# Performance work log

Hardware: AMD Instinct MI355X
Metric: run time of the kernel (lower is better)

The kernel has to match this reference:

```python
import jax, jax.numpy as jnp
import numpy as np

SH, SW = 24, 24       # superpixel grid (num_spixels = 576)
R = 2                 # window_size=5 -> r=2
TEMP = 0.01
N_ITERS = 5
BIG = 1e16


def setup_inputs() -> dict:
    key = jax.random.key(0)
    pixel_features = jax.random.normal(key, (8, 96, 96, 384), dtype=jnp.float32)
    return {"pixel_features": pixel_features}


def _pairwise_dist(f1, f2):
    # f1: (B, C, N) pixels, f2: (B, C, M) superpixels -> (B, M, N)
    return (jnp.sum(f1 * f1, axis=1)[:, None, :]
            + jnp.sum(f2 * f2, axis=1)[:, :, None]
            - 2.0 * jnp.einsum('bcm,bcn->bmn', f2, f1))


def reference(pixel_features):
    B, H, W, C = pixel_features.shape
    M = SH * SW
    x = jnp.transpose(pixel_features, (0, 3, 1, 2))  # (B, C, H, W)

    # init centroids: adaptive_avg_pool2d with divisible dims == block mean
    cent = x.reshape(B, C, SH, H // SH, SW, W // SW).mean(axis=(3, 5)).reshape(B, C, M)

    # nearest-neighbor upsampled label map (same for all batches)
    row = (jnp.arange(H) * SH) // H  # floor(i*SH/H), matches torch 'nearest'
    col = (jnp.arange(W) * SW) // W
    label_map = (row[:, None] * SW + col[None, :]).reshape(-1)  # (N,)

    spix = jnp.arange(M)
    rel_w = label_map[None, :] % SW - spix[:, None] % SW        # (M, N)
    rel_h = label_map[None, :] // SW - spix[:, None] // SW
    mask = (jnp.abs(rel_w) <= R) & (jnp.abs(rel_h) <= R)
    mask_dist = jnp.where(mask, 0.0, BIG).astype(jnp.float32)   # (M, N)

    pix = x.reshape(B, C, H * W)                # (B, C, N)
    pixT = jnp.transpose(pix, (0, 2, 1))        # (B, N, C)

    sp = cent
    for _ in range(N_ITERS):
        d = _pairwise_dist(pix, sp) + mask_dist[None]          # (B, M, N)
        aff = jax.lax.stop_gradient(jax.nn.softmax(-d * TEMP, axis=1))
        sp_new = jnp.einsum('bmn,bnc->bmc', aff, pixT)          # (B, M, C)
        sp_new = sp_new / jnp.maximum(aff.sum(axis=2, keepdims=True), 1e-16)
        sp = jnp.transpose(sp_new, (0, 2, 1))                   # (B, C, M)

    d = _pairwise_dist(pix, sp)
    hard_labels = jnp.argmin(d, axis=1)                         # (B, N)
    spixel_features = jnp.transpose(sp, (0, 2, 1)).reshape(B, SH, SW, C)
    return spixel_features, hard_labels
```

## Files before the change

### kernel.cpp

```cpp
#include <hip/hip_runtime.h>

#define B_ 8
#define H_ 96
#define W_ 96
#define C_ 384
#define SH_ 24
#define SW_ 24
#define M_ 576
#define N_ 9216
#define TEMP_ 0.01f

__global__ __launch_bounds__(384) void k_init(const float* __restrict__ pix,
                                              float* __restrict__ sp,
                                              float* __restrict__ sq) {
  int bm = blockIdx.x;
  int b = bm / M_, m = bm % M_;
  int mh = m / SW_, mw = m % SW_;
  int c = threadIdx.x;
  const float* base = pix + (((size_t)(b * H_ + mh * 4)) * W_ + mw * 4) * C_ + c;
  float s = 0.f;
#pragma unroll
  for (int i = 0; i < 4; i++)
#pragma unroll
    for (int j = 0; j < 4; j++)
      s += base[(size_t)(i * W_ + j) * C_];
  s *= 0.0625f;
  sp[((size_t)(b * M_) + m) * C_ + c] = s;
  float q = s * s;
#pragma unroll
  for (int off = 32; off > 0; off >>= 1) q += __shfl_down(q, off);
  __shared__ float red[6];
  if ((c & 63) == 0) red[c >> 6] = q;
  __syncthreads();
  if (c == 0) sq[b * M_ + m] = red[0] + red[1] + red[2] + red[3] + red[4] + red[5];
}

__global__ __launch_bounds__(128) void k_aff(const float* __restrict__ pix,
                                             const float* __restrict__ sp,
                                             const float* __restrict__ sq,
                                             float* __restrict__ aff) {
  int wg = blockIdx.x;
  int b = wg / 72, r = wg % 72;
  int lh = r / 3, lw0 = (r % 3) * 8;
  __shared__ float sL[60 * 196];
  __shared__ float sqL[60];
  int t = threadIdx.x;
  for (int e = t; e < 60; e += 128) {
    int mh = lh - 2 + e / 12, mw = lw0 - 2 + e % 12;
    sqL[e] = (mh >= 0 && mh < SH_ && mw >= 0 && mw < SW_) ? sq[b * M_ + mh * SW_ + mw] : 0.f;
  }
  int i = t >> 4, j = t & 15;
  int lw = lw0 + i;
  int h = lh * 4 + (j >> 2), w = lw * 4 + (j & 3);
  const float* prow = pix + (((size_t)(b * H_ + h)) * W_ + w) * C_;
  float acc[25];
#pragma unroll
  for (int k = 0; k < 25; k++) acc[k] = 0.f;

  for (int half = 0; half < 2; half++) {
    __syncthreads();
    int cbase = half * 192;
    for (int e = t; e < 60 * 48; e += 128) {
      int u = e / 48, c4 = e % 48;
      int mh = lh - 2 + u / 12, mw = lw0 - 2 + u % 12;
      float4 v = make_float4(0.f, 0.f, 0.f, 0.f);
      if (mh >= 0 && mh < SH_ && mw >= 0 && mw < SW_)
        v = *(const float4*)(sp + ((size_t)(b * M_ + mh * SW_ + mw)) * C_ + cbase + c4 * 4);
      *(float4*)&sL[u * 196 + c4 * 4] = v;
    }
    __syncthreads();
    for (int c0 = 0; c0 < 192; c0 += 8) {
      float4 pa = *(const float4*)(prow + cbase + c0);
      float4 pb = *(const float4*)(prow + cbase + c0 + 4);
#pragma unroll
      for (int dh = 0; dh < 5; dh++) {
#pragma unroll
        for (int dw = 0; dw < 5; dw++) {
          const float* srow = &sL[(dh * 12 + i + dw) * 196 + c0];
          float4 sa = *(const float4*)srow;
          float4 sb = *(const float4*)(srow + 4);
          float tsum = fmaf(pa.x, sa.x, fmaf(pa.y, sa.y, fmaf(pa.z, sa.z, pa.w * sa.w)));
          tsum = fmaf(pb.x, sb.x, fmaf(pb.y, sb.y, fmaf(pb.z, sb.z, fmaf(pb.w, sb.w, tsum))));
          acc[dh * 5 + dw] += tsum;
        }
      }
    }
  }
  float lg[25];
  float mx = -3e38f;
#pragma unroll
  for (int dh = 0; dh < 5; dh++) {
#pragma unroll
    for (int dw = 0; dw < 5; dw++) {
      int k = dh * 5 + dw;
      int mh = lh - 2 + dh, mw = lw - 2 + dw;
      int u = dh * 12 + i + dw;
      bool valid = (mh >= 0) && (mh < SH_) && (mw >= 0) && (mw < SW_);
      float l = valid ? (TEMP_ * (2.f * acc[k] - sqL[u])) : -3e38f;
      lg[k] = l;
      mx = fmaxf(mx, l);
    }
  }
  float z = 0.f;
#pragma unroll
  for (int k = 0; k < 25; k++) {
    float e = __expf(lg[k] - mx);
    lg[k] = e;
    z += e;
  }
  float inv = 1.f / z;
  float* arow = aff + ((size_t)(b * N_) + h * W_ + w) * 25;
#pragma unroll
  for (int k = 0; k < 25; k++) arow[k] = lg[k] * inv;
}

__global__ __launch_bounds__(384) void k_scatter(const float* __restrict__ pix,
                                                 const float* __restrict__ aff,
                                                 float* __restrict__ accum) {
  int wg = blockIdx.x;
  int b = wg / 48, r = wg % 48;
  int lh = r / 2, lw0 = (r % 2) * 12;
  int c = threadIdx.x;
  float acc[5][16];
#pragma unroll
  for (int a = 0; a < 5; a++)
#pragma unroll
    for (int w2 = 0; w2 < 16; w2++) acc[a][w2] = 0.f;
#pragma unroll
  for (int lwl = 0; lwl < 12; lwl++) {
    int lw = lw0 + lwl;
#pragma unroll 4
    for (int jj = 0; jj < 16; jj++) {
      int h = lh * 4 + (jj >> 2);
      int w = lw * 4 + (jj & 3);
      const float* ar = aff + ((size_t)(b * N_) + h * W_ + w) * 25;
      float val = pix[(((size_t)(b * H_) + h) * W_ + w) * C_ + c];
#pragma unroll
      for (int dh = 0; dh < 5; dh++)
#pragma unroll
        for (int dw = 0; dw < 5; dw++)
          acc[dh][lwl + dw] = fmaf(ar[dh * 5 + dw], val, acc[dh][lwl + dw]);
    }
  }
#pragma unroll
  for (int dh = 0; dh < 5; dh++) {
    int mh = lh - 2 + dh;
    if (mh < 0 || mh >= SH_) continue;
#pragma unroll
    for (int wi = 0; wi < 16; wi++) {
      int mw = lw0 - 2 + wi;
      if (mw < 0 || mw >= SW_) continue;
      atomicAdd(&accum[((size_t)(b * M_) + mh * SW_ + mw) * C_ + c], acc[dh][wi]);
    }
  }
}

__global__ __launch_bounds__(384) void k_fin(const float* __restrict__ aff,
                                             const float* __restrict__ accum,
                                             float* __restrict__ sp,
                                             float* __restrict__ sq) {
  int bm = blockIdx.x;
  int b = bm / M_, m = bm % M_;
  int mh = m / SW_, mw = m % SW_;
  int t = threadIdx.x;
  int h0 = (mh - 2) * 4; if (h0 < 0) h0 = 0;
  int h1 = (mh + 3) * 4; if (h1 > H_) h1 = H_;
  int w0 = (mw - 2) * 4; if (w0 < 0) w0 = 0;
  int w1 = (mw + 3) * 4; if (w1 > W_) w1 = W_;
  int nw = w1 - w0;
  int np = (h1 - h0) * nw;
  float d = 0.f;
  for (int e = t; e < np; e += 384) {
    int hh = h0 + e / nw, ww = w0 + e % nw;
    int k = (mh - (hh >> 2) + 2) * 5 + (mw - (ww >> 2) + 2);
    d += aff[((size_t)(b * N_) + hh * W_ + ww) * 25 + k];
  }
  __shared__ float red[6];
#pragma unroll
  for (int off = 32; off > 0; off >>= 1) d += __shfl_down(d, off);
  if ((t & 63) == 0) red[t >> 6] = d;
  __syncthreads();
  float denom = fmaxf(red[0] + red[1] + red[2] + red[3] + red[4] + red[5], 1e-16f);
  size_t idx = ((size_t)(b * M_) + m) * C_ + t;
  float sv = accum[idx] / denom;
  sp[idx] = sv;
  float q = sv * sv;
#pragma unroll
  for (int off = 32; off > 0; off >>= 1) q += __shfl_down(q, off);
  __syncthreads();
  if ((t & 63) == 0) red[t >> 6] = q;
  __syncthreads();
  if (t == 0) sq[b * M_ + m] = red[0] + red[1] + red[2] + red[3] + red[4] + red[5];
}

__global__ __launch_bounds__(256) void k_argmin(const float* __restrict__ pix,
                                                const float* __restrict__ sp,
                                                const float* __restrict__ sq,
                                                float* __restrict__ lab) {
  int wg = blockIdx.x;
  int b = wg / 72;
  int px0 = (wg % 72) * 128;
  __shared__ float pT[128 * 36];
  __shared__ float sT[64 * 36];
  __shared__ float sqT[64];
  int t = threadIdx.x;
  int pxg = t >> 4, cg = t & 15;
  float best[8];
  int bidx[8];
#pragma unroll
  for (int x = 0; x < 8; x++) { best[x] = 3.4e38f; bidx[x] = 0; }

  for (int m0 = 0; m0 < M_; m0 += 64) {
    __syncthreads();
    if (t < 64) sqT[t] = sq[b * M_ + m0 + t];
    float acc[8][4];
#pragma unroll
    for (int x = 0; x < 8; x++)
#pragma unroll
      for (int y = 0; y < 4; y++) acc[x][y] = 0.f;

    for (int k0 = 0; k0 < C_; k0 += 32) {
      __syncthreads();
      {
        int row = t >> 1, o = (t & 1) * 16;
        const float* src = pix + ((size_t)(b * N_) + px0 + row) * C_ + k0 + o;
        int sw = (row >> 3) & 7;
#pragma unroll
        for (int jj = 0; jj < 4; jj++) {
          float4 v = *(const float4*)(src + jj * 4);
          int ob = (o >> 2) + jj;
          *(float4*)&pT[row * 36 + ((ob ^ sw) << 2)] = v;
        }
      }
      if (t < 128) {
        int row = t >> 1, o = (t & 1) * 16;
        const float* src = sp + ((size_t)(b * M_) + m0 + row) * C_ + k0 + o;
        int sw = (row >> 2) & 7;
#pragma unroll
        for (int jj = 0; jj < 4; jj++) {
          float4 v = *(const float4*)(src + jj * 4);
          int ob = (o >> 2) + jj;
          *(float4*)&sT[row * 36 + ((ob ^ sw) << 2)] = v;
        }
      }
      __syncthreads();
#pragma unroll
      for (int q = 0; q < 8; q++) {
        float4 bb[4];
#pragma unroll
        for (int y = 0; y < 4; y++) {
          int row = (cg << 2) + y;
          bb[y] = *(const float4*)&sT[row * 36 + ((q ^ (cg & 7)) << 2)];
        }
#pragma unroll
        for (int x = 0; x < 8; x++) {
          int row = (pxg << 3) + x;
          float4 av = *(const float4*)&pT[row * 36 + ((q ^ (pxg & 7)) << 2)];
#pragma unroll
          for (int y = 0; y < 4; y++) {
            acc[x][y] = fmaf(av.x, bb[y].x,
                        fmaf(av.y, bb[y].y,
                        fmaf(av.z, bb[y].z,
                        fmaf(av.w, bb[y].w, acc[x][y]))));
          }
        }
      }
    }
#pragma unroll
    for (int y = 0; y < 4; y++) {
      int mi = m0 + (cg << 2) + y;
      float dq = sqT[(cg << 2) + y];
#pragma unroll
      for (int x = 0; x < 8; x++) {
        float dist = dq - 2.f * acc[x][y];
        if (dist < best[x]) { best[x] = dist; bidx[x] = mi; }
      }
    }
  }
#pragma unroll
  for (int off = 1; off < 16; off <<= 1) {
#pragma unroll
    for (int x = 0; x < 8; x++) {
      float ov = __shfl_xor(best[x], off, 16);
      int oi = __shfl_xor(bidx[x], off, 16);
      if (ov < best[x] || (ov == best[x] && oi < bidx[x])) { best[x] = ov; bidx[x] = oi; }
    }
  }
  if (cg == 0) {
#pragma unroll
    for (int x = 0; x < 8; x++)
      lab[(size_t)(b * N_) + px0 + (pxg << 3) + x] = (float)bidx[x];
  }
}

__global__ __launch_bounds__(256) void k_copy(const float4* __restrict__ src,
                                              float4* __restrict__ dst) {
  int i = blockIdx.x * 256 + threadIdx.x;
  dst[i] = src[i];
}

extern "C" void kernel_launch(void* const* d_in, const int* in_sizes, int n_in,
                              void* d_out, int out_size, void* d_ws, size_t ws_size,
                              hipStream_t stream) {
  const float* pix = (const float*)d_in[0];
  float* out = (float*)d_out;
  char* ws = (char*)d_ws;
  float* sp    = (float*)(ws);
  float* accum = (float*)(ws + 7077888);
  float* aff   = (float*)(ws + 14155776);
  float* sq    = (float*)(ws + 21528576);

  k_init<<<B_ * M_, 384, 0, stream>>>(pix, sp, sq);
  for (int it = 0; it < 5; it++) {
    hipMemsetAsync(accum, 0, 7077888, stream);
    k_aff<<<576, 128, 0, stream>>>(pix, sp, sq, aff);
    k_scatter<<<384, 384, 0, stream>>>(pix, aff, accum);
    k_fin<<<B_ * M_, 384, 0, stream>>>(aff, accum, sp, sq);
  }
  k_argmin<<<576, 256, 0, stream>>>(pix, sp, sq, out + 1769472);
  k_copy<<<1728, 256, 0, stream>>>((const float4*)sp, (float4*)out);
}
```

Baseline: 1.742 ms.

## Split affinity and argmin kernels across channels and centroids with atomic reduction

The affinity kernel becomes k_dot, which splits the channel dimension into four quarters and processes two pixels per thread across a full superpixel row. Partial dot products are combined into a zeroed buffer with atomicAdd, and a separate k_soft kernel then applies the softmax. The final argmin is split over centroid tiles of 128, giving five times more blocks, and each block merges its result through a 64-bit atomicMin on a packed (distance, index) key held in the output buffer. A k_label pass then unpacks the indices. This raises parallelism for the two compute-heavy stages, at the cost of atomic traffic, an extra memset region and two extra launches.

After: 3.273 ms. 87.9% more time.

```diff
diff --git a/kernel.cpp b/kernel.cpp
--- a/kernel.cpp
+++ b/kernel.cpp
@@ -12,7 +12,10 @@
 
 __global__ __launch_bounds__(384) void k_init(const float* __restrict__ pix,
                                               float* __restrict__ sp,
-                                              float* __restrict__ sq) {
+                                              float* __restrict__ sq,
+                                              unsigned long long* __restrict__ lab64) {
+  int gid = blockIdx.x * 384 + threadIdx.x;
+  if (gid < N_ * B_) lab64[gid] = ~0ull;
   int bm = blockIdx.x;
   int b = bm / M_, m = bm % M_;
   int mh = m / SW_, mw = m % SW_;
@@ -35,68 +38,93 @@
   if (c == 0) sq[b * M_ + m] = red[0] + red[1] + red[2] + red[3] + red[4] + red[5];
 }
 
-__global__ __launch_bounds__(128) void k_aff(const float* __restrict__ pix,
+#define DOT8(ACC, A, BV, SA, SB)                                              \
+  ACC = fmaf((A).x, (SA).x, fmaf((A).y, (SA).y, fmaf((A).z, (SA).z,           \
+        fmaf((A).w, (SA).w, fmaf((BV).x, (SB).x, fmaf((BV).y, (SB).y,         \
+        fmaf((BV).z, (SB).z, fmaf((BV).w, (SB).w, ACC))))))))
+
+__global__ __launch_bounds__(192) void k_dot(const float* __restrict__ pix,
                                              const float* __restrict__ sp,
-                                             const float* __restrict__ sq,
-                                             float* __restrict__ aff) {
+                                             float* __restrict__ dotb) {
   int wg = blockIdx.x;
-  int b = wg / 72, r = wg % 72;
-  int lh = r / 3, lw0 = (r % 3) * 8;
-  __shared__ float sL[60 * 196];
-  __shared__ float sqL[60];
+  int b = wg / 96, r = wg % 96;
+  int lh = r >> 2, quarter = r & 3;
+  int qb = quarter * 96;
+  __shared__ float sL[120 * 52];
   int t = threadIdx.x;
-  for (int e = t; e < 60; e += 128) {
-    int mh = lh - 2 + e / 12, mw = lw0 - 2 + e % 12;
-    sqL[e] = (mh >= 0 && mh < SH_ && mw >= 0 && mw < SW_) ? sq[b * M_ + mh * SW_ + mw] : 0.f;
-  }
-  int i = t >> 4, j = t & 15;
-  int lw = lw0 + i;
-  int h = lh * 4 + (j >> 2), w = lw * 4 + (j & 3);
-  const float* prow = pix + (((size_t)(b * H_ + h)) * W_ + w) * C_;
-  float acc[25];
-#pragma unroll
-  for (int k = 0; k < 25; k++) acc[k] = 0.f;
-
-  for (int half = 0; half < 2; half++) {
+  int lw = t >> 3, pp = t & 7;
+  int h1 = lh * 4 + (pp >> 2), w1 = lw * 4 + (pp & 3);
+  int h2 = h1 + 2;
+  const float* p1 = pix + (((size_t)(b * H_ + h1)) * W_ + w1) * C_ + qb;
+  const float* p2 = pix + (((size_t)(b * H_ + h2)) * W_ + w1) * C_ + qb;
+  int mwc[5];
+#pragma unroll
+  for (int dw = 0; dw < 5; dw++) {
+    int v = lw - 2 + dw;
+    mwc[dw] = v < 0 ? 0 : (v > 23 ? 23 : v);
+  }
+  float acc0[25], acc1[25];
+#pragma unroll
+  for (int k = 0; k < 25; k++) { acc0[k] = 0.f; acc1[k] = 0.f; }
+
+  for (int stg = 0; stg < 2; stg++) {
     __syncthreads();
-    int cbase = half * 192;
-    for (int e = t; e < 60 * 48; e += 128) {
-      int u = e / 48, c4 = e % 48;
-      int mh = lh - 2 + u / 12, mw = lw0 - 2 + u % 12;
+    int cb = stg * 48;
+    for (int e = t; e < 120 * 12; e += 192) {
+      int u = e / 12, c4 = e % 12;
+      int mh = lh - 2 + u / 24, mw = u % 24;
       float4 v = make_float4(0.f, 0.f, 0.f, 0.f);
-      if (mh >= 0 && mh < SH_ && mw >= 0 && mw < SW_)
-        v = *(const float4*)(sp + ((size_t)(b * M_ + mh * SW_ + mw)) * C_ + cbase + c4 * 4);
-      *(float4*)&sL[u * 196 + c4 * 4] = v;
+      if (mh >= 0 && mh < SH_)
+        v = *(const float4*)(sp + ((size_t)(b * M_ + mh * SW_ + mw)) * C_ + qb + cb + c4 * 4);
+      *(float4*)&sL[u * 52 + c4 * 4] = v;
     }
     __syncthreads();
-    for (int c0 = 0; c0 < 192; c0 += 8) {
-      float4 pa = *(const float4*)(prow + cbase + c0);
-      float4 pb = *(const float4*)(prow + cbase + c0 + 4);
+    for (int c0 = 0; c0 < 48; c0 += 8) {
+      float4 a0 = *(const float4*)(p1 + cb + c0);
+      float4 b0 = *(const float4*)(p1 + cb + c0 + 4);
+      float4 a1 = *(const float4*)(p2 + cb + c0);
+      float4 b1 = *(const float4*)(p2 + cb + c0 + 4);
 #pragma unroll
       for (int dh = 0; dh < 5; dh++) {
 #pragma unroll
         for (int dw = 0; dw < 5; dw++) {
-          const float* srow = &sL[(dh * 12 + i + dw) * 196 + c0];
+          const float* srow = &sL[(dh * 24 + mwc[dw]) * 52 + c0];
           float4 sa = *(const float4*)srow;
           float4 sb = *(const float4*)(srow + 4);
-          float tsum = fmaf(pa.x, sa.x, fmaf(pa.y, sa.y, fmaf(pa.z, sa.z, pa.w * sa.w)));
-          tsum = fmaf(pb.x, sb.x, fmaf(pb.y, sb.y, fmaf(pb.z, sb.z, fmaf(pb.w, sb.w, tsum))));
-          acc[dh * 5 + dw] += tsum;
+          int k = dh * 5 + dw;
+          DOT8(acc0[k], a0, b0, sa, sb);
+          DOT8(acc1[k], a1, b1, sa, sb);
         }
       }
     }
   }
+  float* d1 = dotb + ((size_t)(b * N_) + h1 * W_ + w1) * 25;
+  float* d2 = dotb + ((size_t)(b * N_) + h2 * W_ + w1) * 25;
+#pragma unroll
+  for (int k = 0; k < 25; k++) {
+    atomicAdd(d1 + k, acc0[k]);
+    atomicAdd(d2 + k, acc1[k]);
+  }
+}
+
+__global__ __launch_bounds__(256) void k_soft(float* __restrict__ buf,
+                                              const float* __restrict__ sq) {
+  int gid = blockIdx.x * 256 + threadIdx.x;
+  int b = gid / N_, rem = gid % N_;
+  int h = rem / W_, w = rem % W_;
+  int lh = h >> 2, lw = w >> 2;
+  float* row = buf + (size_t)gid * 25;
   float lg[25];
-  float mx = -3e38f;
+  float mx = -3.0e38f;
 #pragma unroll
   for (int dh = 0; dh < 5; dh++) {
 #pragma unroll
     for (int dw = 0; dw < 5; dw++) {
       int k = dh * 5 + dw;
-      int mh = lh - 2 + dh, mw = lw - 2 + dw;
-      int u = dh * 12 + i + dw;
+      int mh = lh + dh - 2, mw = lw + dw - 2;
       bool valid = (mh >= 0) && (mh < SH_) && (mw >= 0) && (mw < SW_);
-      float l = valid ? (TEMP_ * (2.f * acc[k] - sqL[u])) : -3e38f;
+      float l = -3.0e38f;
+      if (valid) l = TEMP_ * (2.f * row[k] - sq[b * M_ + mh * SW_ + mw]);
       lg[k] = l;
       mx = fmaxf(mx, l);
     }
@@ -109,9 +137,8 @@
     z += e;
   }
   float inv = 1.f / z;
-  float* arow = aff + ((size_t)(b * N_) + h * W_ + w) * 25;
-#pragma unroll
-  for (int k = 0; k < 25; k++) arow[k] = lg[k] * inv;
+#pragma unroll
+  for (int k = 0; k < 25; k++) row[k] = lg[k] * inv;
 }
 
 __global__ __launch_bounds__(384) void k_scatter(const float* __restrict__ pix,
@@ -196,85 +223,74 @@
 __global__ __launch_bounds__(256) void k_argmin(const float* __restrict__ pix,
                                                 const float* __restrict__ sp,
                                                 const float* __restrict__ sq,
-                                                float* __restrict__ lab) {
+                                                unsigned long long* __restrict__ lab64) {
   int wg = blockIdx.x;
-  int b = wg / 72;
-  int px0 = (wg % 72) * 128;
+  int b = wg / 360;
+  int r = wg % 360;
+  int px0 = (r / 5) * 128;
+  int m0 = (r % 5) * 128;
   __shared__ float pT[128 * 36];
-  __shared__ float sT[64 * 36];
-  __shared__ float sqT[64];
+  __shared__ float sT[128 * 36];
+  __shared__ float sqT[128];
   int t = threadIdx.x;
   int pxg = t >> 4, cg = t & 15;
+  if (t < 128) {
+    int mm = m0 + t;
+    sqT[t] = (mm < M_) ? sq[b * M_ + mm] : 3.0e38f;
+  }
+  float acc[8][8];
+#pragma unroll
+  for (int x = 0; x < 8; x++)
+#pragma unroll
+    for (int y = 0; y < 8; y++) acc[x][y] = 0.f;
+
+  int srow_ = t >> 1, so_ = (t & 1) * 16;
+  int ssw_ = (srow_ >> 3) & 7;
+  int mrow_ = m0 + srow_; if (mrow_ > M_ - 1) mrow_ = M_ - 1;
+  const float* psrc0 = pix + ((size_t)(b * N_) + px0 + srow_) * C_ + so_;
+  const float* ssrc0 = sp + ((size_t)(b * M_) + mrow_) * C_ + so_;
+
+  for (int k0 = 0; k0 < C_; k0 += 32) {
+    __syncthreads();
+#pragma unroll
+    for (int jj = 0; jj < 4; jj++) {
+      float4 v = *(const float4*)(psrc0 + k0 + jj * 4);
+      float4 u = *(const float4*)(ssrc0 + k0 + jj * 4);
+      int ob = (so_ >> 2) + jj;
+      *(float4*)&pT[srow_ * 36 + (((ob ^ ssw_) & 7) << 2)] = v;
+      *(float4*)&sT[srow_ * 36 + (((ob ^ ssw_) & 7) << 2)] = u;
+    }
+    __syncthreads();
+#pragma unroll
+    for (int q = 0; q < 8; q++) {
+      float4 bb[8];
+      int sb = (q ^ (cg & 7)) << 2;
+#pragma unroll
+      for (int y = 0; y < 8; y++)
+        bb[y] = *(const float4*)&sT[(cg * 8 + y) * 36 + sb];
+      int pb = (q ^ (pxg & 7)) << 2;
+#pragma unroll
+      for (int x = 0; x < 8; x++) {
+        float4 av = *(const float4*)&pT[(pxg * 8 + x) * 36 + pb];
+#pragma unroll
+        for (int y = 0; y < 8; y++)
+          acc[x][y] = fmaf(av.x, bb[y].x, fmaf(av.y, bb[y].y,
+                      fmaf(av.z, bb[y].z, fmaf(av.w, bb[y].w, acc[x][y]))));
+      }
+    }
+  }
   float best[8];
   int bidx[8];
 #pragma unroll
   for (int x = 0; x < 8; x++) { best[x] = 3.4e38f; bidx[x] = 0; }
-
-  for (int m0 = 0; m0 < M_; m0 += 64) {
-    __syncthreads();
-    if (t < 64) sqT[t] = sq[b * M_ + m0 + t];
-    float acc[8][4];
-#pragma unroll
-    for (int x = 0; x < 8; x++)
-#pragma unroll
-      for (int y = 0; y < 4; y++) acc[x][y] = 0.f;
-
-    for (int k0 = 0; k0 < C_; k0 += 32) {
-      __syncthreads();
-      {
-        int row = t >> 1, o = (t & 1) * 16;
-        const float* src = pix + ((size_t)(b * N_) + px0 + row) * C_ + k0 + o;
-        int sw = (row >> 3) & 7;
-#pragma unroll
-        for (int jj = 0; jj < 4; jj++) {
-          float4 v = *(const float4*)(src + jj * 4);
-          int ob = (o >> 2) + jj;
-          *(float4*)&pT[row * 36 + ((ob ^ sw) << 2)] = v;
-        }
-      }
-      if (t < 128) {
-        int row = t >> 1, o = (t & 1) * 16;
-        const float* src = sp + ((size_t)(b * M_) + m0 + row) * C_ + k0 + o;
-        int sw = (row >> 2) & 7;
-#pragma unroll
-        for (int jj = 0; jj < 4; jj++) {
-          float4 v = *(const float4*)(src + jj * 4);
-          int ob = (o >> 2) + jj;
-          *(float4*)&sT[row * 36 + ((ob ^ sw) << 2)] = v;
-        }
-      }
-      __syncthreads();
-#pragma unroll
-      for (int q = 0; q < 8; q++) {
-        float4 bb[4];
-#pragma unroll
-        for (int y = 0; y < 4; y++) {
-          int row = (cg << 2) + y;
-          bb[y] = *(const float4*)&sT[row * 36 + ((q ^ (cg & 7)) << 2)];
-        }
-#pragma unroll
-        for (int x = 0; x < 8; x++) {
-          int row = (pxg << 3) + x;
-          float4 av = *(const float4*)&pT[row * 36 + ((q ^ (pxg & 7)) << 2)];
-#pragma unroll
-          for (int y = 0; y < 4; y++) {
-            acc[x][y] = fmaf(av.x, bb[y].x,
-                        fmaf(av.y, bb[y].y,
-                        fmaf(av.z, bb[y].z,
-                        fmaf(av.w, bb[y].w, acc[x][y]))));
-          }
-        }
-      }
-    }
-#pragma unroll
-    for (int y = 0; y < 4; y++) {
-      int mi = m0 + (cg << 2) + y;
-      float dq = sqT[(cg << 2) + y];
-#pragma unroll
-      for (int x = 0; x < 8; x++) {
-        float dist = dq - 2.f * acc[x][y];
-        if (dist < best[x]) { best[x] = dist; bidx[x] = mi; }
-      }
+#pragma unroll
+  for (int y = 0; y < 8; y++) {
+    int m = m0 + cg * 8 + y;
+    float dq = sqT[cg * 8 + y];
+#pragma unroll
+    for (int x = 0; x < 8; x++) {
+      float d = dq - 2.f * acc[x][y];
+      if (d < best[x]) { best[x] = d; bidx[x] = m; }
     }
   }
 #pragma unroll
@@ -288,9 +304,19 @@
   }
   if (cg == 0) {
 #pragma unroll
-    for (int x = 0; x < 8; x++)
-      lab[(size_t)(b * N_) + px0 + (pxg << 3) + x] = (float)bidx[x];
-  }
+    for (int x = 0; x < 8; x++) {
+      unsigned u = __float_as_uint(best[x]);
+      unsigned k32 = (u & 0x80000000u) ? ~u : (u | 0x80000000u);
+      unsigned long long key = ((unsigned long long)k32 << 32) | (unsigned)bidx[x];
+      atomicMin(lab64 + (size_t)b * N_ + px0 + pxg * 8 + x, key);
+    }
+  }
+}
+
+__global__ __launch_bounds__(256) void k_label(const unsigned long long* __restrict__ lab64,
+                                               float* __restrict__ lab) {
+  int i = blockIdx.x * 256 + threadIdx.x;
+  lab[i] = (float)(unsigned)(lab64[i] & 0xFFFFFFFFull);
 }
 
 __global__ __launch_bounds__(256) void k_copy(const float4* __restrict__ src,
@@ -307,16 +333,19 @@
   char* ws = (char*)d_ws;
   float* sp    = (float*)(ws);
   float* accum = (float*)(ws + 7077888);
-  float* aff   = (float*)(ws + 14155776);
+  float* buf   = (float*)(ws + 14155776);
   float* sq    = (float*)(ws + 21528576);
-
-  k_init<<<B_ * M_, 384, 0, stream>>>(pix, sp, sq);
+  unsigned long long* lab64 = (unsigned long long*)d_out;
+
+  k_init<<<B_ * M_, 384, 0, stream>>>(pix, sp, sq, lab64);
   for (int it = 0; it < 5; it++) {
-    hipMemsetAsync(accum, 0, 7077888, stream);
-    k_aff<<<576, 128, 0, stream>>>(pix, sp, sq, aff);
-    k_scatter<<<384, 384, 0, stream>>>(pix, aff, accum);
-    k_fin<<<B_ * M_, 384, 0, stream>>>(aff, accum, sp, sq);
-  }
-  k_argmin<<<576, 256, 0, stream>>>(pix, sp, sq, out + 1769472);
+    hipMemsetAsync(accum, 0, 7077888 + 7372800, stream);
+    k_dot<<<768, 192, 0, stream>>>(pix, sp, buf);
+    k_soft<<<288, 256, 0, stream>>>(buf, sq);
+    k_scatter<<<384, 384, 0, stream>>>(pix, buf, accum);
+    k_fin<<<B_ * M_, 384, 0, stream>>>(buf, accum, sp, sq);
+  }
+  k_argmin<<<2880, 256, 0, stream>>>(pix, sp, sq, lab64);
+  k_label<<<288, 256, 0, stream>>>(lab64, out + 1769472);
   k_copy<<<1728, 256, 0, stream>>>((const float4*)sp, (float4*)out);
 }
```

## Split argmin over superpixel tiles with 64-bit atomicMin and shrink k_aff LDS

Applied to the files above, without the earlier changes.

k_argmin now splits the superpixel dimension into 5 tiles of 128, so it launches 2880 workgroups instead of 576. It uses 8x8 register tiles per thread with register-prefetch double buffering, and merges partial argmins through a 64-bit atomicMin on packed (distance key, index) values. A new k_label kernel unpacks those keys into float labels, and k_init clears the 64-bit buffer, which lives temporarily in the output area. k_aff stages centroid data in 48-channel chunks instead of 192, cutting its shared memory to raise occupancy at the cost of more barriers. Risks: the atomic traffic, the extra pass, and the 64-bit buffer aliasing the output region that k_copy writes later.

Measured after the change: 1.744 ms. About the same (+0.1%).

```diff
diff --git a/kernel.cpp b/kernel.cpp
--- a/kernel.cpp
+++ b/kernel.cpp
@@ -12,7 +12,10 @@
 
 __global__ __launch_bounds__(384) void k_init(const float* __restrict__ pix,
                                               float* __restrict__ sp,
-                                              float* __restrict__ sq) {
+                                              float* __restrict__ sq,
+                                              unsigned long long* __restrict__ lab64) {
+  int gid = blockIdx.x * 384 + threadIdx.x;
+  if (gid < N_ * B_) lab64[gid] = ~0ull;
   int bm = blockIdx.x;
   int b = bm / M_, m = bm % M_;
   int mh = m / SW_, mw = m % SW_;
@@ -42,7 +45,7 @@
   int wg = blockIdx.x;
   int b = wg / 72, r = wg % 72;
   int lh = r / 3, lw0 = (r % 3) * 8;
-  __shared__ float sL[60 * 196];
+  __shared__ float sL[60 * 52];
   __shared__ float sqL[60];
   int t = threadIdx.x;
   for (int e = t; e < 60; e += 128) {
@@ -57,26 +60,27 @@
 #pragma unroll
   for (int k = 0; k < 25; k++) acc[k] = 0.f;
 
-  for (int half = 0; half < 2; half++) {
+  for (int chunk = 0; chunk < 8; chunk++) {
+    int cb = chunk * 48;
     __syncthreads();
-    int cbase = half * 192;
-    for (int e = t; e < 60 * 48; e += 128) {
-      int u = e / 48, c4 = e % 48;
+    for (int e = t; e < 60 * 12; e += 128) {
+      int u = e / 12, c4 = e % 12;
       int mh = lh - 2 + u / 12, mw = lw0 - 2 + u % 12;
       float4 v = make_float4(0.f, 0.f, 0.f, 0.f);
       if (mh >= 0 && mh < SH_ && mw >= 0 && mw < SW_)
-        v = *(const float4*)(sp + ((size_t)(b * M_ + mh * SW_ + mw)) * C_ + cbase + c4 * 4);
-      *(float4*)&sL[u * 196 + c4 * 4] = v;
+        v = *(const float4*)(sp + ((size_t)(b * M_ + mh * SW_ + mw)) * C_ + cb + c4 * 4);
+      *(float4*)&sL[u * 52 + c4 * 4] = v;
     }
     __syncthreads();
-    for (int c0 = 0; c0 < 192; c0 += 8) {
-      float4 pa = *(const float4*)(prow + cbase + c0);
-      float4 pb = *(const float4*)(prow + cbase + c0 + 4);
+#pragma unroll
+    for (int c0 = 0; c0 < 48; c0 += 8) {
+      float4 pa = *(const float4*)(prow + cb + c0);
+      float4 pb = *(const float4*)(prow + cb + c0 + 4);
 #pragma unroll
       for (int dh = 0; dh < 5; dh++) {
 #pragma unroll
         for (int dw = 0; dw < 5; dw++) {
-          const float* srow = &sL[(dh * 12 + i + dw) * 196 + c0];
+          const float* srow = &sL[(dh * 12 + i + dw) * 52 + c0];
           float4 sa = *(const float4*)srow;
           float4 sb = *(const float4*)(srow + 4);
           float tsum = fmaf(pa.x, sa.x, fmaf(pa.y, sa.y, fmaf(pa.z, sa.z, pa.w * sa.w)));
@@ -196,101 +200,118 @@
 __global__ __launch_bounds__(256) void k_argmin(const float* __restrict__ pix,
                                                 const float* __restrict__ sp,
                                                 const float* __restrict__ sq,
-                                                float* __restrict__ lab) {
+                                                unsigned long long* __restrict__ lab64) {
   int wg = blockIdx.x;
-  int b = wg / 72;
-  int px0 = (wg % 72) * 128;
+  int b = wg / 360;
+  int r = wg % 360;
+  int px0 = (r / 5) * 128;
+  int m0 = (r % 5) * 128;
   __shared__ float pT[128 * 36];
-  __shared__ float sT[64 * 36];
-  __shared__ float sqT[64];
+  __shared__ float sT[128 * 36];
+  __shared__ float sqT[128];
   int t = threadIdx.x;
-  int pxg = t >> 4, cg = t & 15;
+  int wave = t >> 6, lane = t & 63;
+  int wpx = wave >> 1, wc = wave & 1;
+  int pxg = lane >> 3, cg = lane & 7;
+  if (t < 128) {
+    int mm = m0 + t;
+    sqT[t] = (mm < M_) ? sq[b * M_ + mm] : 3.0e38f;
+  }
+  int srow = t >> 1;
+  int sslot0 = (t & 1) * 4;
+  int ssw = (srow >> 3) & 7;
+  int mrow = m0 + srow; if (mrow > M_ - 1) mrow = M_ - 1;
+  const float* psrc = pix + ((size_t)(b * N_) + px0 + srow) * C_ + sslot0 * 4;
+  const float* ssrc = sp + ((size_t)(b * M_) + mrow) * C_ + sslot0 * 4;
+  float* pdst = &pT[srow * 36];
+  float* sdst = &sT[srow * 36];
+
+  float acc[8][8];
+#pragma unroll
+  for (int x = 0; x < 8; x++)
+#pragma unroll
+    for (int y = 0; y < 8; y++) acc[x][y] = 0.f;
+
+  float4 pr[4], sr[4];
+#pragma unroll
+  for (int jj = 0; jj < 4; jj++) {
+    pr[jj] = *(const float4*)(psrc + jj * 4);
+    sr[jj] = *(const float4*)(ssrc + jj * 4);
+  }
+
+  for (int k0 = 0; k0 < C_; k0 += 32) {
+    __syncthreads();
+#pragma unroll
+    for (int jj = 0; jj < 4; jj++) {
+      int slot = (sslot0 + jj) ^ ssw;
+      *(float4*)&pdst[slot << 2] = pr[jj];
+      *(float4*)&sdst[slot << 2] = sr[jj];
+    }
+    __syncthreads();
+    if (k0 + 32 < C_) {
+#pragma unroll
+      for (int jj = 0; jj < 4; jj++) {
+        pr[jj] = *(const float4*)(psrc + k0 + 32 + jj * 4);
+        sr[jj] = *(const float4*)(ssrc + k0 + 32 + jj * 4);
+      }
+    }
+#pragma unroll
+    for (int q = 0; q < 8; q++) {
+      float4 bb[8];
+      int sb = (q ^ cg) << 2;
+#pragma unroll
+      for (int y = 0; y < 8; y++)
+        bb[y] = *(const float4*)&sT[(wc * 64 + cg * 8 + y) * 36 + sb];
+      int pb = (q ^ pxg) << 2;
+#pragma unroll
+      for (int x = 0; x < 8; x++) {
+        float4 av = *(const float4*)&pT[(wpx * 64 + pxg * 8 + x) * 36 + pb];
+#pragma unroll
+        for (int y = 0; y < 8; y++)
+          acc[x][y] = fmaf(av.x, bb[y].x, fmaf(av.y, bb[y].y,
+                      fmaf(av.z, bb[y].z, fmaf(av.w, bb[y].w, acc[x][y]))));
+      }
+    }
+  }
   float best[8];
   int bidx[8];
 #pragma unroll
   for (int x = 0; x < 8; x++) { best[x] = 3.4e38f; bidx[x] = 0; }
-
-  for (int m0 = 0; m0 < M_; m0 += 64) {
-    __syncthreads();
-    if (t < 64) sqT[t] = sq[b * M_ + m0 + t];
-    float acc[8][4];
-#pragma unroll
-    for (int x = 0; x < 8; x++)
-#pragma unroll
-      for (int y = 0; y < 4; y++) acc[x][y] = 0.f;
-
-    for (int k0 = 0; k0 < C_; k0 += 32) {
-      __syncthreads();
-      {
-        int row = t >> 1, o = (t & 1) * 16;
-        const float* src = pix + ((size_t)(b * N_) + px0 + row) * C_ + k0 + o;
-        int sw = (row >> 3) & 7;
-#pragma unroll
-        for (int jj = 0; jj < 4; jj++) {
-          float4 v = *(const float4*)(src + jj * 4);
-          int ob = (o >> 2) + jj;
-          *(float4*)&pT[row * 36 + ((ob ^ sw) << 2)] = v;
-        }
-      }
-      if (t < 128) {
-        int row = t >> 1, o = (t & 1) * 16;
-        const float* src = sp + ((size_t)(b * M_) + m0 + row) * C_ + k0 + o;
-        int sw = (row >> 2) & 7;
-#pragma unroll
-        for (int jj = 0; jj < 4; jj++) {
-          float4 v = *(const float4*)(src + jj * 4);
-          int ob = (o >> 2) + jj;
-          *(float4*)&sT[row * 36 + ((ob ^ sw) << 2)] = v;
-        }
-      }
-      __syncthreads();
-#pragma unroll
-      for (int q = 0; q < 8; q++) {
-        float4 bb[4];
-#pragma unroll
-        for (int y = 0; y < 4; y++) {
-          int row = (cg << 2) + y;
-          bb[y] = *(const float4*)&sT[row * 36 + ((q ^ (cg & 7)) << 2)];
-        }
-#pragma unroll
-        for (int x = 0; x < 8; x++) {
-          int row = (pxg << 3) + x;
-          float4 av = *(const float4*)&pT[row * 36 + ((q ^ (pxg & 7)) << 2)];
-#pragma unroll
-          for (int y = 0; y < 4; y++) {
-            acc[x][y] = fmaf(av.x, bb[y].x,
-                        fmaf(av.y, bb[y].y,
-                        fmaf(av.z, bb[y].z,
-                        fmaf(av.w, bb[y].w, acc[x][y]))));
-          }
-        }
-      }
-    }
-#pragma unroll
-    for (int y = 0; y < 4; y++) {
-      int mi = m0 + (cg << 2) + y;
-      float dq = sqT[(cg << 2) + y];
-#pragma unroll
-      for (int x = 0; x < 8; x++) {
-        float dist = dq - 2.f * acc[x][y];
-        if (dist < best[x]) { best[x] = dist; bidx[x] = mi; }
-      }
-    }
-  }
-#pragma unroll
-  for (int off = 1; off < 16; off <<= 1) {
+#pragma unroll
+  for (int y = 0; y < 8; y++) {
+    int lc = wc * 64 + cg * 8 + y;
+    int mi = m0 + lc;
+    float dq = sqT[lc];
 #pragma unroll
     for (int x = 0; x < 8; x++) {
-      float ov = __shfl_xor(best[x], off, 16);
-      int oi = __shfl_xor(bidx[x], off, 16);
+      float d = dq - 2.f * acc[x][y];
+      if (d < best[x]) { best[x] = d; bidx[x] = mi; }
+    }
+  }
+#pragma unroll
+  for (int off = 1; off < 8; off <<= 1) {
+#pragma unroll
+    for (int x = 0; x < 8; x++) {
+      float ov = __shfl_xor(best[x], off);
+      int oi = __shfl_xor(bidx[x], off);
       if (ov < best[x] || (ov == best[x] && oi < bidx[x])) { best[x] = ov; bidx[x] = oi; }
     }
   }
   if (cg == 0) {
 #pragma unroll
-    for (int x = 0; x < 8; x++)
-      lab[(size_t)(b * N_) + px0 + (pxg << 3) + x] = (float)bidx[x];
-  }
+    for (int x = 0; x < 8; x++) {
+      unsigned u = __float_as_uint(best[x]);
+      unsigned k32 = (u & 0x80000000u) ? ~u : (u | 0x80000000u);
+      unsigned long long key = ((unsigned long long)k32 << 32) | (unsigned)bidx[x];
+      atomicMin(lab64 + (size_t)b * N_ + px0 + wpx * 64 + pxg * 8 + x, key);
+    }
+  }
+}
+
+__global__ __launch_bounds__(256) void k_label(const unsigned long long* __restrict__ lab64,
+                                               float* __restrict__ lab) {
+  int i = blockIdx.x * 256 + threadIdx.x;
+  lab[i] = (float)(unsigned)(lab64[i] & 0xFFFFFFFFull);
 }
 
 __global__ __launch_bounds__(256) void k_copy(const float4* __restrict__ src,
@@ -309,14 +330,16 @@
   float* accum = (float*)(ws + 7077888);
   float* aff   = (float*)(ws + 14155776);
   float* sq    = (float*)(ws + 21528576);
-
-  k_init<<<B_ * M_, 384, 0, stream>>>(pix, sp, sq);
+  unsigned long long* lab64 = (unsigned long long*)d_out;
+
+  k_init<<<B_ * M_, 384, 0, stream>>>(pix, sp, sq, lab64);
   for (int it = 0; it < 5; it++) {
     hipMemsetAsync(accum, 0, 7077888, stream);
     k_aff<<<576, 128, 0, stream>>>(pix, sp, sq, aff);
     k_scatter<<<384, 384, 0, stream>>>(pix, aff, accum);
     k_fin<<<B_ * M_, 384, 0, stream>>>(aff, accum, sp, sq);
   }
-  k_argmin<<<576, 256, 0, stream>>>(pix, sp, sq, out + 1769472);
+  k_argmin<<<2880, 256, 0, stream>>>(pix, sp, sq, lab64);
+  k_label<<<288, 256, 0, stream>>>(lab64, out + 1769472);
   k_copy<<<1728, 256, 0, stream>>>((const float4*)sp, (float4*)out);
 }
```
